# Kernel optimization log

Measured on AMD Instinct MI355X. Metric: run time of the kernel, lower is better.

## Reference

```python
import jax, jax.numpy as jnp
import numpy as np

S = 14
B = 2
C = 20
LAMBDA_COORD = 5.0
LAMBDA_NOOBJ = 0.5
BATCH = 4096


def setup_inputs() -> dict:
    key = jax.random.key(0)
    k1, k2, k3 = jax.random.split(key, 3)
    pred = jax.random.uniform(k1, (BATCH, S, S, B * 5 + C), dtype=jnp.float32)
    target = jax.random.uniform(k2, (BATCH, S, S, B * 5 + C), dtype=jnp.float32)
    obj = (jax.random.uniform(k3, (BATCH, S, S), dtype=jnp.float32) < 0.15).astype(jnp.float32)
    target = target.at[..., 4].set(obj)
    target = target.at[..., 9].set(obj)
    return {"pred": pred, "target": target}


def _iou(box1, box2):
    # box1, box2: (..., 4) = [x, y, w, h]; elementwise IoU over leading dims
    b1x1 = box1[..., 0] - box1[..., 2] / 2
    b1y1 = box1[..., 1] - box1[..., 3] / 2
    b1x2 = box1[..., 0] + box1[..., 2] / 2
    b1y2 = box1[..., 1] + box1[..., 3] / 2
    b2x1 = box2[..., 0] - box2[..., 2] / 2
    b2y1 = box2[..., 1] - box2[..., 3] / 2
    b2x2 = box2[..., 0] + box2[..., 2] / 2
    b2y2 = box2[..., 1] + box2[..., 3] / 2
    iw = jnp.clip(jnp.minimum(b1x2, b2x2) - jnp.maximum(b1x1, b2x1), 0)
    ih = jnp.clip(jnp.minimum(b1y2, b2y2) - jnp.maximum(b1y1, b2y1), 0)
    inter = iw * ih
    a1 = (b1x2 - b1x1) * (b1y2 - b1y1)
    a2 = (b2x2 - b2x1) * (b2y2 - b2y1)
    return inter / (a1 + a2 - inter + 1e-6)


def reference(pred, target):
    bs = pred.shape[0]
    tb = target[..., : B * 5].reshape(bs, S, S, B, 5)
    pb = pred[..., : B * 5].reshape(bs, S, S, B, 5)
    tcls = target[..., B * 5 :]
    pcls = pred[..., B * 5 :]

    obj_mask = tb[..., 4] > 0          # (bs,S,S,B)
    has_obj = obj_mask[..., 0]         # (bs,S,S)
    noobj_mask = ~obj_mask

    # no-object confidence loss over every non-obj box slot
    conf_err2 = (pb[..., 4] - tb[..., 4]) ** 2
    noobj_loss = jnp.sum(jnp.where(noobj_mask, conf_err2, 0.0))

    # per-box IoU between i-th pred box and i-th target box in each cell
    ious = _iou(pb[..., :4], tb[..., :4])            # (bs,S,S,B)
    best_idx = jnp.argmax(ious, axis=-1)             # (bs,S,S)
    idx = best_idx[..., None, None]
    p_best = jnp.take_along_axis(pb, idx, axis=3)[..., 0, :]  # (bs,S,S,5)
    t_best = jnp.take_along_axis(tb, idx, axis=3)[..., 0, :]

    m = has_obj                                       # (bs,S,S) bool
    mf = m.astype(pred.dtype)

    xy_loss = jnp.sum(mf[..., None] * (p_best[..., :2] - t_best[..., :2]) ** 2)
    p_wh = jnp.sqrt(jnp.abs(p_best[..., 2:4]) + 1e-6)
    t_wh_safe = jnp.where(m[..., None], t_best[..., 2:4], 1.0)  # avoid sqrt(0) grad NaN
    t_wh = jnp.sqrt(t_wh_safe)
    wh_loss = jnp.sum(mf[..., None] * (p_wh - t_wh) ** 2)
    coord_loss = xy_loss + wh_loss

    obj_loss = jnp.sum(mf * (p_best[..., 4] - t_best[..., 4]) ** 2)

    # non-best box confidence pushed to 0 (B=2: the other slot)
    nonbest_conf = jnp.sum(pb[..., 4], axis=-1) - p_best[..., 4]
    noobj_loss = noobj_loss + LAMBDA_NOOBJ * jnp.sum(mf * nonbest_conf ** 2)

    class_loss = jnp.sum(mf[..., None] * (pcls - tcls) ** 2)

    total = LAMBDA_COORD * coord_loss + obj_loss + LAMBDA_NOOBJ * noobj_loss + class_loss
    return total / bs
```

## Files before the change

### kernel.cpp

```cpp
#include <hip/hip_runtime.h>


#define FEAT 30
#define CELLS 802816
#define TPB 256
#define CPB 256
#define NBLOCKS (CELLS / CPB)
#define F4_PER_TILE (CPB * FEAT / 4)

__device__ __forceinline__ float iou_f(float x1, float y1, float w1, float h1,
                                       float x2, float y2, float w2, float h2) {
    float b1x1 = x1 - 0.5f * w1, b1x2 = x1 + 0.5f * w1;
    float b1y1 = y1 - 0.5f * h1, b1y2 = y1 + 0.5f * h1;
    float b2x1 = x2 - 0.5f * w2, b2x2 = x2 + 0.5f * w2;
    float b2y1 = y2 - 0.5f * h2, b2y2 = y2 + 0.5f * h2;
    float iw = fmaxf(fminf(b1x2, b2x2) - fmaxf(b1x1, b2x1), 0.0f);
    float ih = fmaxf(fminf(b1y2, b2y2) - fmaxf(b1y1, b2y1), 0.0f);
    float inter = iw * ih;
    float a1 = (b1x2 - b1x1) * (b1y2 - b1y1);
    float a2 = (b2x2 - b2x1) * (b2y2 - b2y1);
    return inter / (a1 + a2 - inter + 1e-6f);
}

__global__ __launch_bounds__(TPB) void yolo_main_kernel(
        const float* __restrict__ pred, const float* __restrict__ tgt,
        float* __restrict__ partials) {
    __shared__ float sp[CPB * FEAT];
    __shared__ float st[CPB * FEAT];
    __shared__ float wave_sum[TPB / 64];

    const int tid = threadIdx.x;
    const long long base = (long long)blockIdx.x * (CPB * FEAT);

    const float4* gp = (const float4*)(pred + base);
    const float4* gt = (const float4*)(tgt + base);
    float4* lp = (float4*)sp;
    float4* lt = (float4*)st;
#pragma unroll
    for (int i = 0; i < 7; ++i) {
        lp[tid + i * TPB] = gp[tid + i * TPB];
        lt[tid + i * TPB] = gt[tid + i * TPB];
    }
    if (tid < (F4_PER_TILE - 7 * TPB)) {
        lp[tid + 7 * TPB] = gp[tid + 7 * TPB];
        lt[tid + 7 * TPB] = gt[tid + 7 * TPB];
    }
    __syncthreads();

    float p[FEAT], t[FEAT];
    const float2* pc = (const float2*)(sp + tid * FEAT);
    const float2* tc = (const float2*)(st + tid * FEAT);
#pragma unroll
    for (int i = 0; i < FEAT / 2; ++i) {
        float2 vp = pc[i]; p[2 * i] = vp.x; p[2 * i + 1] = vp.y;
        float2 vt = tc[i]; t[2 * i] = vt.x; t[2 * i + 1] = vt.y;
    }

    const bool obj0 = t[4] > 0.0f;
    const bool obj1 = t[9] > 0.0f;
    const float mf = obj0 ? 1.0f : 0.0f;

    float d0 = p[4] - t[4];
    float d1 = p[9] - t[9];
    float noobj = (obj0 ? 0.0f : d0 * d0) + (obj1 ? 0.0f : d1 * d1);

    float iou0 = iou_f(p[0], p[1], p[2], p[3], t[0], t[1], t[2], t[3]);
    float iou1 = iou_f(p[5], p[6], p[7], p[8], t[5], t[6], t[7], t[8]);
    const bool sel1 = iou1 > iou0;

    float pbx = sel1 ? p[5] : p[0];
    float pby = sel1 ? p[6] : p[1];
    float pbw = sel1 ? p[7] : p[2];
    float pbh = sel1 ? p[8] : p[3];
    float pbc = sel1 ? p[9] : p[4];
    float tbx = sel1 ? t[5] : t[0];
    float tby = sel1 ? t[6] : t[1];
    float tbw = sel1 ? t[7] : t[2];
    float tbh = sel1 ? t[8] : t[3];
    float tbc = sel1 ? t[9] : t[4];

    float dx = pbx - tbx, dy = pby - tby;
    float xy = dx * dx + dy * dy;

    float pw = sqrtf(fabsf(pbw) + 1e-6f);
    float ph = sqrtf(fabsf(pbh) + 1e-6f);
    float tw = sqrtf(obj0 ? tbw : 1.0f);
    float th = sqrtf(obj0 ? tbh : 1.0f);
    float dw = pw - tw, dh = ph - th;
    float wh = dw * dw + dh * dh;

    float dc = pbc - tbc;
    float obj_l = dc * dc;

    float nonbest = (p[4] + p[9]) - pbc;
    noobj += 0.5f * mf * nonbest * nonbest;

    float cls = 0.0f;
#pragma unroll
    for (int k = 10; k < FEAT; ++k) {
        float d = p[k] - t[k];
        cls += d * d;
    }

    float cell = 5.0f * mf * (xy + wh) + mf * obj_l + 0.5f * noobj + mf * cls;

    float v = cell;
#pragma unroll
    for (int off = 32; off > 0; off >>= 1) v += __shfl_down(v, off, 64);
    __syncthreads();
    if ((tid & 63) == 0) wave_sum[tid >> 6] = v;
    __syncthreads();
    if (tid == 0)
        partials[blockIdx.x] = wave_sum[0] + wave_sum[1] + wave_sum[2] + wave_sum[3];
}

__global__ __launch_bounds__(TPB) void yolo_reduce_kernel(
        const float* __restrict__ partials, float* __restrict__ out) {
    __shared__ float wave_sum[TPB / 64];
    const int tid = threadIdx.x;
    float v = 0.0f;
    for (int i = tid; i < NBLOCKS; i += TPB) v += partials[i];
#pragma unroll
    for (int off = 32; off > 0; off >>= 1) v += __shfl_down(v, off, 64);
    if ((tid & 63) == 0) wave_sum[tid >> 6] = v;
    __syncthreads();
    if (tid == 0)
        out[0] = (wave_sum[0] + wave_sum[1] + wave_sum[2] + wave_sum[3]) *
                 (1.0f / 4096.0f);
}

extern "C" void kernel_launch(void* const* d_in, const int* in_sizes, int n_in,
                              void* d_out, int out_size, void* d_ws, size_t ws_size,
                              hipStream_t stream) {
    const float* pred = (const float*)d_in[0];
    const float* tgt  = (const float*)d_in[1];
    float* out = (float*)d_out;
    float* partials = (float*)d_ws;

    yolo_main_kernel<<<NBLOCKS, TPB, 0, stream>>>(pred, tgt, partials);
    yolo_reduce_kernel<<<1, TPB, 0, stream>>>(partials, out);
}
```

Baseline: 206.6 us.

## Load cell pairs directly via float4, drop LDS staging, fuse reduction with atomics

Each thread now handles two adjacent cells (60 floats, 16-byte aligned), loading them straight from global memory with float4 reads into registers instead of staging tiles through shared memory. The second reduce kernel is removed; each block atomically adds its scaled partial sum to the output, which is zeroed with a memset. This removes the LDS round trip, a barrier and a kernel launch. In exchange, per-thread strided float4 loads are less coalesced, register pressure rises, and float atomics make the summation order nondeterministic.

```diff
diff --git a/kernel.cpp b/kernel.cpp
--- a/kernel.cpp
+++ b/kernel.cpp
@@ -3,10 +3,9 @@
 
 #define FEAT 30
 #define CELLS 802816
+#define PAIRS (CELLS / 2)
 #define TPB 256
-#define CPB 256
-#define NBLOCKS (CELLS / CPB)
-#define F4_PER_TILE (CPB * FEAT / 4)
+#define NB (PAIRS / TPB)
 
 __device__ __forceinline__ float iou_f(float x1, float y1, float w1, float h1,
                                        float x2, float y2, float w2, float h2) {
@@ -22,40 +21,7 @@
     return inter / (a1 + a2 - inter + 1e-6f);
 }
 
-__global__ __launch_bounds__(TPB) void yolo_main_kernel(
-        const float* __restrict__ pred, const float* __restrict__ tgt,
-        float* __restrict__ partials) {
-    __shared__ float sp[CPB * FEAT];
-    __shared__ float st[CPB * FEAT];
-    __shared__ float wave_sum[TPB / 64];
-
-    const int tid = threadIdx.x;
-    const long long base = (long long)blockIdx.x * (CPB * FEAT);
-
-    const float4* gp = (const float4*)(pred + base);
-    const float4* gt = (const float4*)(tgt + base);
-    float4* lp = (float4*)sp;
-    float4* lt = (float4*)st;
-#pragma unroll
-    for (int i = 0; i < 7; ++i) {
-        lp[tid + i * TPB] = gp[tid + i * TPB];
-        lt[tid + i * TPB] = gt[tid + i * TPB];
-    }
-    if (tid < (F4_PER_TILE - 7 * TPB)) {
-        lp[tid + 7 * TPB] = gp[tid + 7 * TPB];
-        lt[tid + 7 * TPB] = gt[tid + 7 * TPB];
-    }
-    __syncthreads();
-
-    float p[FEAT], t[FEAT];
-    const float2* pc = (const float2*)(sp + tid * FEAT);
-    const float2* tc = (const float2*)(st + tid * FEAT);
-#pragma unroll
-    for (int i = 0; i < FEAT / 2; ++i) {
-        float2 vp = pc[i]; p[2 * i] = vp.x; p[2 * i + 1] = vp.y;
-        float2 vt = tc[i]; t[2 * i] = vt.x; t[2 * i + 1] = vt.y;
-    }
-
+__device__ __forceinline__ float cell_loss(const float* p, const float* t) {
     const bool obj0 = t[4] > 0.0f;
     const bool obj1 = t[9] > 0.0f;
     const float mf = obj0 ? 1.0f : 0.0f;
@@ -102,31 +68,39 @@
         cls += d * d;
     }
 
-    float cell = 5.0f * mf * (xy + wh) + mf * obj_l + 0.5f * noobj + mf * cls;
-
-    float v = cell;
-#pragma unroll
-    for (int off = 32; off > 0; off >>= 1) v += __shfl_down(v, off, 64);
-    __syncthreads();
-    if ((tid & 63) == 0) wave_sum[tid >> 6] = v;
-    __syncthreads();
-    if (tid == 0)
-        partials[blockIdx.x] = wave_sum[0] + wave_sum[1] + wave_sum[2] + wave_sum[3];
+    return 5.0f * mf * (xy + wh) + mf * obj_l + 0.5f * noobj + mf * cls;
 }
 
-__global__ __launch_bounds__(TPB) void yolo_reduce_kernel(
-        const float* __restrict__ partials, float* __restrict__ out) {
+__global__ __launch_bounds__(TPB) void yolo_kernel(
+        const float* __restrict__ pred, const float* __restrict__ tgt,
+        float* __restrict__ out) {
     __shared__ float wave_sum[TPB / 64];
+
     const int tid = threadIdx.x;
-    float v = 0.0f;
-    for (int i = tid; i < NBLOCKS; i += TPB) v += partials[i];
+    const long long pair = (long long)blockIdx.x * TPB + tid;
+
+    const float4* gp = (const float4*)(pred + pair * (2 * FEAT));
+    const float4* gt = (const float4*)(tgt + pair * (2 * FEAT));
+
+    float pf[2 * FEAT], tf[2 * FEAT];
+#pragma unroll
+    for (int i = 0; i < 15; ++i) {
+        float4 a = gp[i];
+        pf[4 * i] = a.x; pf[4 * i + 1] = a.y; pf[4 * i + 2] = a.z; pf[4 * i + 3] = a.w;
+        float4 b = gt[i];
+        tf[4 * i] = b.x; tf[4 * i + 1] = b.y; tf[4 * i + 2] = b.z; tf[4 * i + 3] = b.w;
+    }
+
+    float v = cell_loss(pf, tf) + cell_loss(pf + FEAT, tf + FEAT);
+
 #pragma unroll
     for (int off = 32; off > 0; off >>= 1) v += __shfl_down(v, off, 64);
     if ((tid & 63) == 0) wave_sum[tid >> 6] = v;
     __syncthreads();
-    if (tid == 0)
-        out[0] = (wave_sum[0] + wave_sum[1] + wave_sum[2] + wave_sum[3]) *
-                 (1.0f / 4096.0f);
+    if (tid == 0) {
+        float blk = wave_sum[0] + wave_sum[1] + wave_sum[2] + wave_sum[3];
+        atomicAdd(out, blk * (1.0f / 4096.0f));
+    }
 }
 
 extern "C" void kernel_launch(void* const* d_in, const int* in_sizes, int n_in,
@@ -135,8 +109,7 @@
     const float* pred = (const float*)d_in[0];
     const float* tgt  = (const float*)d_in[1];
     float* out = (float*)d_out;
-    float* partials = (float*)d_ws;
 
-    yolo_main_kernel<<<NBLOCKS, TPB, 0, stream>>>(pred, tgt, partials);
-    yolo_reduce_kernel<<<1, TPB, 0, stream>>>(partials, out);
+    hipMemsetAsync(out, 0, sizeof(float), stream);
+    yolo_kernel<<<NB, TPB, 0, stream>>>(pred, tgt, out);
 }
```

Measured after the change: 233.3 us. 12.9% more time.
